# Performance work log

Measured on AMD Instinct MI355X. Metric: run time of the kernel, lower is better.

## Reference

```python
import jax, jax.numpy as jnp
import numpy as np
from jax import lax

T, B, A = 128, 32, 18  # rollout steps, num envs, action dim
HID = 128
FEAT = 512


def _conv(x, w, b, stride):
    y = lax.conv_general_dilated(x, w, (stride, stride), 'VALID',
                                 dimension_numbers=('NCHW', 'OIHW', 'NCHW'))
    return y + b[None, :, None, None]


def setup_inputs() -> dict:
    key = jax.random.key(0)
    ks = jax.random.split(key, 16)

    def w(k, shape, fan_in):
        return jax.random.normal(k, shape, dtype=jnp.float32) / np.sqrt(fan_in)

    x = jax.random.uniform(ks[0], (T * B, 4, 84, 84), dtype=jnp.float32) * 255.0
    done = jax.random.randint(ks[1], (T * B,), 0, 2, dtype=jnp.int32)
    h0 = jax.random.normal(ks[2], (1, B, HID), dtype=jnp.float32) * 0.1
    c0 = jax.random.normal(ks[3], (1, B, HID), dtype=jnp.float32) * 0.1
    return {
        'x': x, 'done': done, 'h0': h0, 'c0': c0,
        'w1': w(ks[4], (32, 4, 8, 8), 4 * 64), 'b1': jnp.zeros((32,), jnp.float32),
        'w2': w(ks[5], (64, 32, 4, 4), 32 * 16), 'b2': jnp.zeros((64,), jnp.float32),
        'w3': w(ks[6], (64, 64, 3, 3), 64 * 9), 'b3': jnp.zeros((64,), jnp.float32),
        'wf': w(ks[7], (FEAT, 3136), 3136), 'bf': jnp.zeros((FEAT,), jnp.float32),
        'w_ih': w(ks[8], (4 * HID, FEAT), FEAT), 'w_hh': w(ks[9], (4 * HID, HID), HID),
        'b_ih': jnp.zeros((4 * HID,), jnp.float32), 'b_hh': jnp.zeros((4 * HID,), jnp.float32),
        'wa': w(ks[10], (A, HID), HID) * 0.01, 'ba': jnp.zeros((A,), jnp.float32),
        'wc': w(ks[11], (1, HID), HID), 'bc': jnp.zeros((1,), jnp.float32),
    }


def reference(x, done, h0, c0, w1, b1, w2, b2, w3, b3, wf, bf,
              w_ih, w_hh, b_ih, b_hh, wa, ba, wc, bc):
    # Nature-CNN trunk on x/255
    h = jax.nn.relu(_conv(x / 255.0, w1, b1, 4))   # (TB,32,20,20)
    h = jax.nn.relu(_conv(h, w2, b2, 2))           # (TB,64,9,9)
    h = jax.nn.relu(_conv(h, w3, b3, 1))           # (TB,64,7,7)
    h = h.reshape(h.shape[0], -1)                   # (TB,3136)
    feat = jax.nn.relu(h @ wf.T + bf)               # (TB,512)

    xs = feat.reshape(T, B, FEAT)
    ds = done.reshape(T, B).astype(feat.dtype)

    def step(carry, inp):
        hh, cc = carry
        xt, dt = inp
        m = (1.0 - dt)[:, None]      # done-mask reset of recurrent state
        hh = hh * m
        cc = cc * m
        gates = xt @ w_ih.T + b_ih + hh @ w_hh.T + b_hh
        i, f, g, o = jnp.split(gates, 4, axis=-1)  # torch LSTM gate order
        cc = jax.nn.sigmoid(f) * cc + jax.nn.sigmoid(i) * jnp.tanh(g)
        hh = jax.nn.sigmoid(o) * jnp.tanh(cc)
        return (hh, cc), hh

    (_, _), hs = lax.scan(step, (h0[0], c0[0]), (xs, ds))
    hidden = hs.reshape(T * B, HID)

    logits = hidden @ wa.T + ba                     # actor head
    value = hidden @ wc.T + bc                      # critic head
    return jnp.concatenate([logits, value], axis=-1)  # (TB, A+1)
```

## Files before the change

### kernel.cpp

```cpp
#include <hip/hip_runtime.h>

typedef _Float16 f16;
typedef _Float16 f16x2 __attribute__((ext_vector_type(2)));
typedef _Float16 f16x4 __attribute__((ext_vector_type(4)));
typedef _Float16 f16x8 __attribute__((ext_vector_type(8)));
typedef float f32x4 __attribute__((ext_vector_type(4)));

__device__ __forceinline__ float sigf(float x){ return 1.f/(1.f + __expf(-x)); }
__device__ __forceinline__ float tanhfast(float x){ return 2.f/(1.f + __expf(-2.f*x)) - 1.f; }
__device__ __forceinline__ float fdot2f(f16x2 a, f16x2 b, float c){
#if __has_builtin(__builtin_amdgcn_fdot2)
  return __builtin_amdgcn_fdot2(a, b, c, false);
#else
  return c + (float)a.x*(float)b.x + (float)a.y*(float)b.y;
#endif
}

__global__ void prep_w1(const float* __restrict__ w, f16* __restrict__ dst){
  int idx = blockIdx.x*256 + threadIdx.x;
  if (idx >= 8192) return;
  int och = idx >> 8, rem = idx & 255;
  int c = rem >> 6, ky = (rem >> 3) & 7, kx = rem & 7;
  int k = c*64 + ky*8 + kx;
  dst[(k>>3)*256 + och*8 + (k&7)] = (f16)(w[idx] * (1.f/255.f));
}
__global__ void prep_w2(const float* __restrict__ w, f16* __restrict__ dst){
  int idx = blockIdx.x*256 + threadIdx.x;
  if (idx >= 32768) return;
  int och = idx >> 9;
  int c = (idx >> 4) & 31, ky = (idx >> 2) & 3, kx = idx & 3;
  int k = (ky*4 + kx)*32 + c;
  dst[(k>>3)*512 + och*8 + (k&7)] = (f16)w[idx];
}
__global__ void prep_w3(const float* __restrict__ w, f16* __restrict__ dst){
  int idx = blockIdx.x*256 + threadIdx.x;
  if (idx >= 36864) return;
  int och = idx / 576, r = idx % 576;
  int c = r / 9, r2 = r % 9;
  int ky = r2 / 3, kx = r2 % 3;
  int k = (ky*3 + kx)*64 + c;
  dst[(k>>3)*512 + och*8 + (k&7)] = (f16)w[idx];
}
__global__ void prep_wf(const float* __restrict__ w, f16* __restrict__ dst){
  int idx = blockIdx.x*256 + threadIdx.x;
  if (idx >= 392*512*8) return;
  int j = idx & 7, n = (idx >> 3) & 511, k8 = idx >> 12;
  int kf = k8*8 + j;
  int c = kf & 63, p = kf >> 6;
  dst[idx] = (f16)w[(size_t)n*3136 + c*49 + p];
}
__global__ void prep_wih(const float* __restrict__ w, f16* __restrict__ dst){
  int idx = blockIdx.x*256 + threadIdx.x;
  if (idx >= 262144) return;
  int j = idx & 7, n = (idx >> 3) & 511, k8 = idx >> 12;
  dst[idx] = (f16)w[n*512 + k8*8 + j];
}
__global__ void prep_wheads(const float* __restrict__ wa, const float* __restrict__ wc,
                            f16* __restrict__ dst){
  int idx = blockIdx.x*256 + threadIdx.x;
  if (idx >= 4096) return;
  int n = idx >> 7, k = idx & 127;
  float v = 0.f;
  if (n < 18) v = wa[n*128 + k];
  else if (n == 18) v = wc[k];
  dst[(k>>3)*256 + n*8 + (k&7)] = (f16)v;
}
__global__ void prep_bsum(const float* __restrict__ a, const float* __restrict__ b,
                          float* __restrict__ s){
  int i = blockIdx.x*256 + threadIdx.x;
  if (i < 512) s[i] = a[i] + b[i];
}
__global__ void prep_whh(const float* __restrict__ w, f16* __restrict__ dst){
  int idx = blockIdx.x*256 + threadIdx.x;
  if (idx >= 65536) return;
  int nn = idx >> 7, k = idx & 127;
  dst[(k >> 1)*1024 + nn*2 + (k & 1)] = (f16)w[idx];
}

__global__ __launch_bounds__(256) void conv123_k(const float* __restrict__ x,
    const f16* __restrict__ Bp1, const float* __restrict__ b1,
    const f16* __restrict__ Bp2, const float* __restrict__ b2,
    const f16* __restrict__ Bp3, const float* __restrict__ b3,
    f16* __restrict__ y3){
  __shared__ alignas(16) f16 xt[4*44*84];
  __shared__ alignas(16) f16 y1t[400*32];
  int n = blockIdx.x;
  int tid = threadIdx.x;
  int lane = tid & 63, w = tid >> 6;
  int q = lane >> 4, m = lane & 15;

  int wg = w & 1, wm = w >> 1;
  int och1 = wg*16 + m;
  f16x8 bfr1[8];
  #pragma unroll
  for (int s = 0; s < 8; ++s)
    bfr1[s] = *(const f16x8*)(Bp1 + ((4*s + q)*32 + och1)*8);
  float bias1 = b1[och1];

  #pragma unroll
  for (int h = 0; h < 2; ++h){
    for (int i = tid; i < 3696; i += 256){
      int c = i / 924, r = i % 924;
      int iy = r / 21, x4 = r % 21;
      const float4* xp = (const float4*)(x + (((size_t)n*4 + c)*84 + h*40 + iy)*84) + x4;
      float4 v = *xp;
      f16x4 hv = { (f16)v.x, (f16)v.y, (f16)v.z, (f16)v.w };
      *(f16x4*)(&xt[(c*44 + iy)*84 + x4*4]) = hv;
    }
    __syncthreads();
    int oy4[7], ox4[7];
    #pragma unroll
    for (int i = 0; i < 7; ++i){
      int pxl = (wm*7 + i)*16 + m; if (pxl > 199) pxl = 199;
      oy4[i] = (pxl/20)*4; ox4[i] = (pxl%20)*4;
    }
    f32x4 acc1[7] = {};
    #pragma unroll
    for (int s = 0; s < 8; ++s){
      int k8 = 4*s + q;
      int c = k8 >> 3, ky = k8 & 7;
      #pragma unroll
      for (int i = 0; i < 7; ++i){
        const f16* ap = &xt[(c*44 + oy4[i] + ky)*84 + ox4[i]];
        f16x4 lo = *(const f16x4*)ap;
        f16x4 hi = *(const f16x4*)(ap + 4);
        f16x8 a = __builtin_shufflevector(lo, hi, 0,1,2,3,4,5,6,7);
        acc1[i] = __builtin_amdgcn_mfma_f32_16x16x32_f16(a, bfr1[s], acc1[i], 0, 0, 0);
      }
    }
    #pragma unroll
    for (int i = 0; i < 7; ++i)
      #pragma unroll
      for (int r = 0; r < 4; ++r){
        int pxl = (wm*7 + i)*16 + q*4 + r;
        if (pxl < 200){
          float v = acc1[i][r] + bias1; v = v > 0.f ? v : 0.f;
          y1t[(h*200 + pxl)*32 + och1] = (f16)v;
        }
      }
    __syncthreads();
  }

  int och2 = w*16 + m;
  f16x8 bfr2[16];
  #pragma unroll
  for (int s = 0; s < 16; ++s)
    bfr2[s] = *(const f16x8*)(Bp2 + ((size_t)(4*s + q)*64 + och2)*8);
  int basev[6];
  #pragma unroll
  for (int i = 0; i < 6; ++i){
    int px = i*16 + m; if (px > 80) px = 80;
    basev[i] = (px/9*2)*20 + (px%9)*2;
  }
  f32x4 acc2[6] = {};
  #pragma unroll
  for (int s = 0; s < 16; ++s){
    int k8 = 4*s + q;
    int c0 = (k8 & 3)*8;
    int kk = k8 >> 2;
    int off = ((kk >> 2)*20 + (kk & 3))*32 + c0;
    #pragma unroll
    for (int i = 0; i < 6; ++i){
      f16x8 a = *(const f16x8*)(&y1t[basev[i]*32 + off]);
      acc2[i] = __builtin_amdgcn_mfma_f32_16x16x32_f16(a, bfr2[s], acc2[i], 0, 0, 0);
    }
  }
  float bias2 = b2[och2];
  #pragma unroll
  for (int i = 0; i < 6; ++i)
    #pragma unroll
    for (int r = 0; r < 4; ++r){
      int px = i*16 + q*4 + r;
      if (px < 81){
        float v = acc2[i][r] + bias2; v = v > 0.f ? v : 0.f;
        xt[px*64 + och2] = (f16)v;
      }
    }
  __syncthreads();

  int basev3[4];
  #pragma unroll
  for (int i = 0; i < 4; ++i){
    int px = i*16 + m; if (px > 48) px = 48;
    basev3[i] = (px/7)*9 + (px%7);
  }
  f32x4 acc3[4] = {};
  for (int s = 0; s < 18; ++s){
    int k8 = 4*s + q;
    int c0 = (k8 & 7)*8;
    int kxy = k8 >> 3;
    int ky = kxy/3, kx = kxy%3;
    f16x8 b = *(const f16x8*)(Bp3 + ((size_t)k8*64 + och2)*8);
    int off = (ky*9 + kx)*64 + c0;
    #pragma unroll
    for (int i = 0; i < 4; ++i){
      f16x8 a = *(const f16x8*)(&xt[basev3[i]*64 + off]);
      acc3[i] = __builtin_amdgcn_mfma_f32_16x16x32_f16(a, b, acc3[i], 0, 0, 0);
    }
  }
  float bias3 = b3[och2];
  #pragma unroll
  for (int i = 0; i < 4; ++i)
    #pragma unroll
    for (int r = 0; r < 4; ++r){
      int px = i*16 + q*4 + r;
      if (px < 49){
        float v = acc3[i][r] + bias3; v = v > 0.f ? v : 0.f;
        y3[((size_t)n*49 + px)*64 + och2] = (f16)v;
      }
    }
}

template<bool RELU, bool OUTH>
__global__ __launch_bounds__(256) void gemm_k(const f16* __restrict__ A,
    const f16* __restrict__ Bp, const float* __restrict__ bias, void* __restrict__ out,
    int M, int N, int K){
  __shared__ alignas(16) f16 at[64*264];
  int m0 = blockIdx.x*64, n0 = blockIdx.y*64;
  int lane = threadIdx.x & 63, w = threadIdx.x >> 6;
  int q = lane >> 4, cl = lane & 15;
  int mh = w >> 1, nh = w & 1;
  f32x4 acc[2][2] = {};
  for (int kb = 0; kb < K; kb += 256){
    int kblen = K - kb; if (kblen > 256) kblen = 256;
    int c8n = kblen >> 3;
    __syncthreads();
    int tot = 64*c8n;
    for (int i = threadIdx.x; i < tot; i += 256){
      int row, c8;
      if (c8n == 32){ row = i >> 5; c8 = i & 31; } else { row = i >> 3; c8 = i & 7; }
      *(f16x8*)(&at[row*264 + c8*8]) = *(const f16x8*)(&A[(size_t)(m0+row)*K + kb + c8*8]);
    }
    __syncthreads();
    int nks = kblen >> 5;
    for (int s = 0; s < nks; ++s){
      f16x8 a[2], b[2];
      #pragma unroll
      for (int mi = 0; mi < 2; ++mi)
        a[mi] = *(const f16x8*)(&at[((mh*2+mi)*16 + cl)*264 + 32*s + 8*q]);
      #pragma unroll
      for (int ni = 0; ni < 2; ++ni){
        int nn = n0 + (nh*2+ni)*16 + cl;
        b[ni] = *(const f16x8*)(&Bp[((size_t)((kb>>3) + 4*s + q)*N + nn)*8]);
      }
      #pragma unroll
      for (int mi = 0; mi < 2; ++mi)
        #pragma unroll
        for (int ni = 0; ni < 2; ++ni)
          acc[mi][ni] = __builtin_amdgcn_mfma_f32_16x16x32_f16(a[mi], b[ni], acc[mi][ni], 0,0,0);
    }
  }
  #pragma unroll
  for (int ni = 0; ni < 2; ++ni){
    int nn = n0 + (nh*2+ni)*16 + cl;
    float bv = bias[nn];
    #pragma unroll
    for (int mi = 0; mi < 2; ++mi)
      #pragma unroll
      for (int r = 0; r < 4; ++r){
        int mg = m0 + (mh*2+mi)*16 + q*4 + r;
        float v = acc[mi][ni][r] + bv;
        if (RELU) v = v > 0.f ? v : 0.f;
        if (OUTH) ((f16*)out)[(size_t)mg*N + nn] = (f16)v;
        else      ((float*)out)[(size_t)mg*N + nn] = v;
      }
  }
}

__global__ __launch_bounds__(128) void lstm_seg(const float* __restrict__ gx,
    const f16* __restrict__ whhT2, const int* __restrict__ done,
    const float* __restrict__ h0, const float* __restrict__ c0,
    f16* __restrict__ hs){
  int e = blockIdx.y, t0 = blockIdx.x;
  if (t0 > 0 && done[t0*32 + e] == 0) return;
  int j = threadIdx.x;
  __shared__ f16 hl[2][128];
  float h, c;
  if (t0 == 0){
    float mm = 1.f - (float)done[e];
    h = h0[e*128 + j]*mm;
    c = c0[e*128 + j]*mm;
  } else { h = 0.f; c = 0.f; }
  int buf = 0;
  hl[0][j] = (f16)h;
  __syncthreads();
  const f16x2* wp = (const f16x2*)whhT2;
  for (int t = t0; t < 128; ++t){
    if (t > t0 && done[t*32 + e] != 0) break;
    const float* gxr = gx + ((size_t)t*32 + e)*512;
    float gi = gxr[j], gf = gxr[128 + j], gg = gxr[256 + j], go = gxr[384 + j];
    const f16x2* hp = (const f16x2*)hl[buf];
    float ai = 0.f, af = 0.f, ag = 0.f, ao = 0.f;
    #pragma unroll 8
    for (int k2 = 0; k2 < 64; ++k2){
      f16x2 hv = hp[k2];
      const f16x2* wr = wp + k2*512;
      ai = fdot2f(wr[j], hv, ai);
      af = fdot2f(wr[128 + j], hv, af);
      ag = fdot2f(wr[256 + j], hv, ag);
      ao = fdot2f(wr[384 + j], hv, ao);
    }
    gi += ai; gf += af; gg += ag; go += ao;
    c = sigf(gf)*c + sigf(gi)*tanhfast(gg);
    h = sigf(go)*tanhfast(c);
    hs[((size_t)t*32 + e)*128 + j] = (f16)h;
    buf ^= 1;
    hl[buf][j] = (f16)h;
    __syncthreads();
  }
}

__global__ __launch_bounds__(256) void heads_k(const f16* __restrict__ hs,
    const f16* __restrict__ Bp, const float* __restrict__ ba, const float* __restrict__ bc,
    float* __restrict__ out){
  __shared__ alignas(16) f16 at[64*128];
  int m0 = blockIdx.x*64;
  for (int i = threadIdx.x; i < 1024; i += 256)
    ((uint4*)at)[i] = ((const uint4*)(hs + (size_t)m0*128))[i];
  int lane = threadIdx.x & 63, w = threadIdx.x >> 6;
  int q = lane >> 4, cl = lane & 15;
  __syncthreads();
  f32x4 acc[2] = {};
  #pragma unroll
  for (int s = 0; s < 4; ++s){
    f16x8 a = *(const f16x8*)(&at[(w*16 + cl)*128 + 32*s + 8*q]);
    #pragma unroll
    for (int nt = 0; nt < 2; ++nt){
      f16x8 b = *(const f16x8*)(&Bp[((4*s + q)*32 + nt*16 + cl)*8]);
      acc[nt] = __builtin_amdgcn_mfma_f32_16x16x32_f16(a, b, acc[nt], 0,0,0);
    }
  }
  #pragma unroll
  for (int nt = 0; nt < 2; ++nt){
    int n = nt*16 + cl;
    if (n < 19){
      float bv = (n < 18) ? ba[n] : bc[0];
      #pragma unroll
      for (int r = 0; r < 4; ++r){
        int m = m0 + w*16 + q*4 + r;
        out[(size_t)m*19 + n] = acc[nt][r] + bv;
      }
    }
  }
}

extern "C" void kernel_launch(void* const* d_in, const int* in_sizes, int n_in,
                              void* d_out, int out_size, void* d_ws, size_t ws_size,
                              hipStream_t stream){
  const float* x   = (const float*)d_in[0];
  const int*   dn  = (const int*)d_in[1];
  const float* h0  = (const float*)d_in[2];
  const float* c0  = (const float*)d_in[3];
  const float* w1  = (const float*)d_in[4];
  const float* b1  = (const float*)d_in[5];
  const float* w2  = (const float*)d_in[6];
  const float* b2  = (const float*)d_in[7];
  const float* w3  = (const float*)d_in[8];
  const float* b3  = (const float*)d_in[9];
  const float* wf  = (const float*)d_in[10];
  const float* bf  = (const float*)d_in[11];
  const float* wih = (const float*)d_in[12];
  const float* whh = (const float*)d_in[13];
  const float* bih = (const float*)d_in[14];
  const float* bhh = (const float*)d_in[15];
  const float* wa  = (const float*)d_in[16];
  const float* ba  = (const float*)d_in[17];
  const float* wc  = (const float*)d_in[18];
  const float* bc  = (const float*)d_in[19];
  float* out = (float*)d_out;

  char* ws = (char*)d_ws;
  size_t off = 0;
  auto alloc = [&](size_t bytes)->char*{
    char* p = ws + off;
    off += (bytes + 255) & ~(size_t)255;
    return p;
  };
  f16*  y3   = (f16*)alloc(4096UL*3136*2);
  f16*  feat = (f16*)alloc(4096UL*512*2);
  float* gx  = (float*)alloc(4096UL*512*4);
  f16*  hs   = (f16*)alloc(4096UL*128*2);
  f16*  Bp1  = (f16*)alloc(32UL*32*8*2);
  f16*  Bp2  = (f16*)alloc(64UL*64*8*2);
  f16*  Bp3  = (f16*)alloc(72UL*64*8*2);
  f16*  Bpf  = (f16*)alloc(392UL*512*8*2);
  f16*  Bpih = (f16*)alloc(64UL*512*8*2);
  f16*  Bph  = (f16*)alloc(16UL*32*8*2);
  float* bsum = (float*)alloc(512UL*4);
  f16*  whhT2 = (f16*)alloc(64UL*512*2*2);

  prep_w1<<<32, 256, 0, stream>>>(w1, Bp1);
  prep_w2<<<128, 256, 0, stream>>>(w2, Bp2);
  prep_w3<<<144, 256, 0, stream>>>(w3, Bp3);
  prep_wf<<<6272, 256, 0, stream>>>(wf, Bpf);
  prep_wih<<<1024, 256, 0, stream>>>(wih, Bpih);
  prep_wheads<<<16, 256, 0, stream>>>(wa, wc, Bph);
  prep_bsum<<<2, 256, 0, stream>>>(bih, bhh, bsum);
  prep_whh<<<256, 256, 0, stream>>>(whh, whhT2);

  conv123_k<<<4096, 256, 0, stream>>>(x, Bp1, b1, Bp2, b2, Bp3, b3, y3);
  gemm_k<true,  true ><<<dim3(64, 8), 256, 0, stream>>>(y3,   Bpf,  bf,   (void*)feat, 4096, 512, 3136);
  gemm_k<false, false><<<dim3(64, 8), 256, 0, stream>>>(feat, Bpih, bsum, (void*)gx,   4096, 512, 512);
  lstm_seg<<<dim3(128, 32), 128, 0, stream>>>(gx, whhT2, dn, h0, c0, hs);
  heads_k<<<64, 256, 0, stream>>>(hs, Bph, ba, bc, out);
}
```

Measured before the change: 948.2 us.

## Shrink conv1 input tile to quarter rows and swizzle LDS layouts

The conv1 input staging tile is cut from two halves of 44 rows to four quarters of 24 rows, which lowers shared memory per block, and launch bounds now request 3 blocks per SM to raise occupancy. The y1t and conv2-output LDS buffers get XOR swizzles on the channel offset to reduce bank conflicts on the f16x8 A-fragment reads in conv2 and conv3. The tradeoff is more sync/load phases, smaller MFMA batches per phase, and register pressure from the occupancy bound.

```diff
diff --git a/kernel.cpp b/kernel.cpp
--- a/kernel.cpp
+++ b/kernel.cpp
@@ -77,12 +77,12 @@
   dst[(k >> 1)*1024 + nn*2 + (k & 1)] = (f16)w[idx];
 }
 
-__global__ __launch_bounds__(256) void conv123_k(const float* __restrict__ x,
+__global__ __launch_bounds__(256, 3) void conv123_k(const float* __restrict__ x,
     const f16* __restrict__ Bp1, const float* __restrict__ b1,
     const f16* __restrict__ Bp2, const float* __restrict__ b2,
     const f16* __restrict__ Bp3, const float* __restrict__ b3,
     f16* __restrict__ y3){
-  __shared__ alignas(16) f16 xt[4*44*84];
+  __shared__ alignas(16) f16 xt[4*24*84];
   __shared__ alignas(16) f16 y1t[400*32];
   int n = blockIdx.x;
   int tid = threadIdx.x;
@@ -98,30 +98,31 @@
   float bias1 = b1[och1];
 
   #pragma unroll
-  for (int h = 0; h < 2; ++h){
-    for (int i = tid; i < 3696; i += 256){
-      int c = i / 924, r = i % 924;
+  for (int h = 0; h < 4; ++h){
+    for (int i = tid; i < 2016; i += 256){
+      int c = i / 504, r = i % 504;
       int iy = r / 21, x4 = r % 21;
-      const float4* xp = (const float4*)(x + (((size_t)n*4 + c)*84 + h*40 + iy)*84) + x4;
+      const float4* xp = (const float4*)(x + (((size_t)n*4 + c)*84 + h*20 + iy)*84) + x4;
       float4 v = *xp;
       f16x4 hv = { (f16)v.x, (f16)v.y, (f16)v.z, (f16)v.w };
-      *(f16x4*)(&xt[(c*44 + iy)*84 + x4*4]) = hv;
+      *(f16x4*)(&xt[(c*24 + iy)*84 + x4*4]) = hv;
     }
     __syncthreads();
-    int oy4[7], ox4[7];
-    #pragma unroll
-    for (int i = 0; i < 7; ++i){
-      int pxl = (wm*7 + i)*16 + m; if (pxl > 199) pxl = 199;
-      oy4[i] = (pxl/20)*4; ox4[i] = (pxl%20)*4;
-    }
-    f32x4 acc1[7] = {};
+    int oy4[4], ox4[4];
+    #pragma unroll
+    for (int i = 0; i < 4; ++i){
+      int pl = i*16 + m; if (pl > 49) pl = 49;
+      int p = wm*50 + pl;
+      oy4[i] = (p/20)*4; ox4[i] = (p%20)*4;
+    }
+    f32x4 acc1[4] = {};
     #pragma unroll
     for (int s = 0; s < 8; ++s){
       int k8 = 4*s + q;
       int c = k8 >> 3, ky = k8 & 7;
       #pragma unroll
-      for (int i = 0; i < 7; ++i){
-        const f16* ap = &xt[(c*44 + oy4[i] + ky)*84 + ox4[i]];
+      for (int i = 0; i < 4; ++i){
+        const f16* ap = &xt[(c*24 + oy4[i] + ky)*84 + ox4[i]];
         f16x4 lo = *(const f16x4*)ap;
         f16x4 hi = *(const f16x4*)(ap + 4);
         f16x8 a = __builtin_shufflevector(lo, hi, 0,1,2,3,4,5,6,7);
@@ -129,13 +130,15 @@
       }
     }
     #pragma unroll
-    for (int i = 0; i < 7; ++i)
+    for (int i = 0; i < 4; ++i)
       #pragma unroll
       for (int r = 0; r < 4; ++r){
-        int pxl = (wm*7 + i)*16 + q*4 + r;
-        if (pxl < 200){
+        int pl = i*16 + q*4 + r;
+        if (pl < 50){
+          int P = h*100 + wm*50 + pl;
           float v = acc1[i][r] + bias1; v = v > 0.f ? v : 0.f;
-          y1t[(h*200 + pxl)*32 + och1] = (f16)v;
+          int idx = (P*32 + och1) ^ (((P>>1)&7)<<3);
+          y1t[idx] = (f16)v;
         }
       }
     __syncthreads();
@@ -158,10 +161,12 @@
     int k8 = 4*s + q;
     int c0 = (k8 & 3)*8;
     int kk = k8 >> 2;
-    int off = ((kk >> 2)*20 + (kk & 3))*32 + c0;
+    int poff = (kk >> 2)*20 + (kk & 3);
     #pragma unroll
     for (int i = 0; i < 6; ++i){
-      f16x8 a = *(const f16x8*)(&y1t[basev[i]*32 + off]);
+      int p = basev[i] + poff;
+      int idx = (p*32 + c0) ^ (((p>>1)&7)<<3);
+      f16x8 a = *(const f16x8*)(&y1t[idx]);
       acc2[i] = __builtin_amdgcn_mfma_f32_16x16x32_f16(a, bfr2[s], acc2[i], 0, 0, 0);
     }
   }
@@ -173,7 +178,8 @@
       int px = i*16 + q*4 + r;
       if (px < 81){
         float v = acc2[i][r] + bias2; v = v > 0.f ? v : 0.f;
-        xt[px*64 + och2] = (f16)v;
+        int idx = (px*64 + och2) ^ ((px&7)<<3);
+        xt[idx] = (f16)v;
       }
     }
   __syncthreads();
@@ -191,10 +197,12 @@
     int kxy = k8 >> 3;
     int ky = kxy/3, kx = kxy%3;
     f16x8 b = *(const f16x8*)(Bp3 + ((size_t)k8*64 + och2)*8);
-    int off = (ky*9 + kx)*64 + c0;
+    int poff = ky*9 + kx;
     #pragma unroll
     for (int i = 0; i < 4; ++i){
-      f16x8 a = *(const f16x8*)(&xt[basev3[i]*64 + off]);
+      int p = basev3[i] + poff;
+      int idx = (p*64 + c0) ^ ((p&7)<<3);
+      f16x8 a = *(const f16x8*)(&xt[idx]);
       acc3[i] = __builtin_amdgcn_mfma_f32_16x16x32_f16(a, b, acc3[i], 0, 0, 0);
     }
   }
```

Measured after the change: 897.6 us. -5.3%, faster.
